# Kernel tuning notes

Measured on AMD Instinct MI355X. Metric: run time of the kernel, lower is better.

The kernel has to match this reference:

```python
import jax, jax.numpy as jnp
from jax import lax
import numpy as np

B, L, D_MODEL = 4, 2048, 1024
D_INNER = 2 * D_MODEL          # expand=2
N = 16                          # d_state
DCONV = 4                       # d_conv
DTRANK = D_MODEL // 16          # dt_rank = 64
DFF = 4 * D_MODEL               # 4096


def setup_inputs() -> dict:
    key = jax.random.key(0)
    ks = jax.random.split(key, 10)
    def g(i, shape, scale=0.02):
        return jax.random.normal(ks[i], shape, jnp.float32) * scale
    return {
        "x": jax.random.normal(ks[0], (B, L, D_MODEL), jnp.float32),
        # Mamba params (mamba_ssm defaults: in_proj/x_proj/out_proj no bias)
        "in_proj_w": g(1, (2 * D_INNER, D_MODEL)),
        "conv_w": g(2, (D_INNER, 1, DCONV), 0.1),
        "conv_b": jnp.zeros((D_INNER,), jnp.float32),
        "x_proj_w": g(3, (DTRANK + 2 * N, D_INNER)),
        "dt_proj_w": g(4, (D_INNER, DTRANK), 0.1),
        # inverse-softplus of ~0.01 so softplus(dt) starts small, as in Mamba init
        "dt_proj_b": jnp.log(jnp.expm1(jnp.full((D_INNER,), 1e-2, jnp.float32))),
        "A_log": jnp.log(jnp.broadcast_to(jnp.arange(1, N + 1, dtype=jnp.float32), (D_INNER, N))),
        "D": jnp.ones((D_INNER,), jnp.float32),
        "out_proj_w": g(5, (D_MODEL, D_INNER)),
        # FFN params (nn.Linear has bias)
        "lin1_w": g(6, (DFF, D_MODEL)),
        "lin1_b": jnp.zeros((DFF,), jnp.float32),
        "lin2_w": g(7, (D_MODEL, DFF)),
        "lin2_b": jnp.zeros((D_MODEL,), jnp.float32),
    }


def _mamba(x, in_proj_w, conv_w, conv_b, x_proj_w, dt_proj_w, dt_proj_b,
           A_log, D, out_proj_w):
    Bb = x.shape[0]
    xz = jnp.einsum('bld,ed->ble', x, in_proj_w)        # [B,L,2*d_inner]
    u, z = jnp.split(xz, 2, axis=-1)                    # each [B,L,d_inner]
    # causal depthwise conv1d over time
    uc = jnp.transpose(u, (0, 2, 1))                    # [B,d_inner,L]
    uc = lax.conv_general_dilated(uc, conv_w, (1,), [(DCONV - 1, 0)],
                                  feature_group_count=D_INNER)
    uc = jax.nn.silu(uc + conv_b[None, :, None])
    u = jnp.transpose(uc, (0, 2, 1))                    # [B,L,d_inner]
    # input-dependent dt, B, C
    x_dbl = jnp.einsum('ble,fe->blf', u, x_proj_w)      # [B,L,dt_rank+2N]
    dt, Bm, Cm = jnp.split(x_dbl, [DTRANK, DTRANK + N], axis=-1)
    dt = jax.nn.softplus(jnp.einsum('blr,er->ble', dt, dt_proj_w) + dt_proj_b)
    A = -jnp.exp(A_log)                                 # [d_inner,N]

    def step(h, inputs):
        u_t, dt_t, B_t, C_t = inputs                    # [B,E],[B,E],[B,N],[B,N]
        dA = jnp.exp(dt_t[..., None] * A)               # [B,E,N]
        h = dA * h + (dt_t * u_t)[..., None] * B_t[:, None, :]
        y = jnp.einsum('ben,bn->be', h, C_t)
        return h, y

    h0 = jnp.zeros((Bb, D_INNER, N), x.dtype)
    xs = (jnp.transpose(u, (1, 0, 2)), jnp.transpose(dt, (1, 0, 2)),
          jnp.transpose(Bm, (1, 0, 2)), jnp.transpose(Cm, (1, 0, 2)))
    _, ys = lax.scan(step, h0, xs)                      # ys: [L,B,d_inner]
    y = jnp.transpose(ys, (1, 0, 2)) + u * D
    y = y * jax.nn.silu(z)
    return jnp.einsum('ble,de->bld', y, out_proj_w)     # [B,L,d_model]


def reference(x, in_proj_w, conv_w, conv_b, x_proj_w, dt_proj_w, dt_proj_b,
              A_log, D, out_proj_w, lin1_w, lin1_b, lin2_w, lin2_b):
    y = _mamba(x, in_proj_w, conv_w, conv_b, x_proj_w, dt_proj_w, dt_proj_b,
               A_log, D, out_proj_w)
    h = jax.nn.relu(jnp.einsum('bld,fd->blf', y, lin1_w) + lin1_b)
    return jnp.einsum('blf,df->bld', h, lin2_w) + lin2_b
```

## Files before the change

### kernel.cpp

```cpp
#include <hip/hip_runtime.h>
#include <hip/hip_bf16.h>
#include <type_traits>
#include <math.h>

typedef __hip_bfloat16 bf16_t;

#define BB 4
#define LL 2048
#define DM 1024
#define DI 2048
#define NS 16
#define DTR 64
#define DFF 4096
#define MTOK (BB*LL)
#define NC 32
#define CL (LL/NC)
#define TT 16
#define KS 4

#if defined(__has_builtin)
#if __has_builtin(__builtin_amdgcn_exp2f)
#define EXP2F(x) __builtin_amdgcn_exp2f(x)
#endif
#endif
#ifndef EXP2F
#define EXP2F(x) exp2f(x)
#endif
#define LOG2E 1.44269504088896340736f

__device__ __forceinline__ float b2f_lo(unsigned u) {
    union { unsigned x; float f; } c; c.x = u << 16; return c.f;
}
__device__ __forceinline__ float b2f_hi(unsigned u) {
    union { unsigned x; float f; } c; c.x = u & 0xffff0000u; return c.f;
}
__device__ __forceinline__ void unpack8(uint4 v, float* o) {
    o[0] = b2f_lo(v.x); o[1] = b2f_hi(v.x);
    o[2] = b2f_lo(v.y); o[3] = b2f_hi(v.y);
    o[4] = b2f_lo(v.z); o[5] = b2f_hi(v.z);
    o[6] = b2f_lo(v.w); o[7] = b2f_hi(v.w);
}

typedef __attribute__((ext_vector_type(8))) short bf16x8;
typedef __attribute__((ext_vector_type(4))) float f32x4;

__device__ __forceinline__ void gld_lds16(const void* g, void* l) {
    __builtin_amdgcn_global_load_lds(
        (const __attribute__((address_space(1))) void*)g,
        (__attribute__((address_space(3))) void*)l, 16, 0, 0);
}

#define G8_BAR  __builtin_amdgcn_s_barrier()
#define G8_SB   __builtin_amdgcn_sched_barrier(0)
#define G8_LGKM do { asm volatile("s_waitcnt lgkmcnt(0)" ::: "memory"); G8_SB; } while (0)
#define G8_VM4  do { asm volatile("s_waitcnt vmcnt(4)"   ::: "memory"); G8_SB; } while (0)
#define G8_VM2  do { asm volatile("s_waitcnt vmcnt(2)"   ::: "memory"); G8_SB; } while (0)
#define G8_VM0  do { asm volatile("s_waitcnt vmcnt(0)"   ::: "memory"); G8_SB; } while (0)

__global__ void detect_dtype_kernel(const unsigned* __restrict__ x, int* __restrict__ flag)
{
    __shared__ int cnt;
    if (threadIdx.x == 0) cnt = 0;
    __syncthreads();
    int c = 0;
    for (int i = threadIdx.x; i < 4096; i += 256) {
        unsigned w = x[i];
        int e = (w >> 7) & 0xFF;
        c += (e >= 100 && e <= 140) ? 1 : 0;
    }
    atomicAdd(&cnt, c);
    __syncthreads();
    if (threadIdx.x == 0) *flag = (cnt > 2048) ? 1 : 0;
}

struct CvtDesc {
    const void* src[14];
    bf16_t*     dst[14];
    int         cum[15];
};

__global__ __launch_bounds__(256)
void convert_all(CvtDesc d, const int* __restrict__ flag, int total8)
{
    int i = blockIdx.x * 256 + threadIdx.x;
    if (i >= total8) return;
    int t = 0;
#pragma unroll 1
    while (i >= d.cum[t + 1]) ++t;
    int j = i - d.cum[t];
    if (*flag) {
        ((uint4*)d.dst[t])[j] = ((const uint4*)d.src[t])[j];
    } else {
        const float4* s = (const float4*)d.src[t] + (size_t)j * 2;
        float4 a = s[0], b = s[1];
        bf16_t o[8];
        o[0] = __float2bfloat16(a.x); o[1] = __float2bfloat16(a.y);
        o[2] = __float2bfloat16(a.z); o[3] = __float2bfloat16(a.w);
        o[4] = __float2bfloat16(b.x); o[5] = __float2bfloat16(b.y);
        o[6] = __float2bfloat16(b.z); o[7] = __float2bfloat16(b.w);
        ((uint4*)d.dst[t])[j] = *(uint4*)o;
    }
}

#define G8_NK 16

template <int EPI, bool SPLIT>
__global__ __launch_bounds__(512, 2)
void gemm8(const bf16_t* __restrict__ A, const bf16_t* __restrict__ W,
           bf16_t* __restrict__ C, bf16_t* __restrict__ C2,
           const bf16_t* __restrict__ bias, int ldc)
{
    __shared__ __align__(16) bf16_t ldsmem[2][2][256 * 64];

    const int tid  = threadIdx.x;
    const int lane = tid & 63;
    const int wv   = tid >> 6;
    const int wm   = wv >> 2;
    const int wn   = wv & 3;
    const int r16  = lane & 15;
    const int q    = lane >> 4;
    const int m0   = blockIdx.x * 256;
    const int n0   = blockIdx.y * 256;

    const int x0 = q ^ (r16 & 7);
    const int x1 = (4 + q) ^ (r16 & 7);

    const int srow = tid >> 3;
    const int scol = (tid & 7) ^ (srow & 7);
    const bf16_t* Abase = A + (size_t)(m0 + srow) * 1024 + scol * 8;
    const bf16_t* Wbase = W + (size_t)(n0 + srow) * 1024 + scol * 8;
    const int woff = wv * 1024;

    const bf16x8* L8 = (const bf16x8*)ldsmem;
    char*         Lb = (char*)ldsmem;

    f32x4  acc[8][4] = {};
    bf16x8 af[4][2];
    bf16x8 bfr[2][2][2];

    auto stA = [&](int bufc, int tile, int half) {
        const bf16_t* g = Abase + (size_t)half * (128 * 1024) + tile * 64;
        char* l = Lb + (size_t)(bufc * 2 + 0) * 32768 + half * 16384 + woff;
        gld_lds16(g, l);
        gld_lds16(g + 64 * 1024, l + 8192);
    };
    auto stB = [&](int bufc, int tile, int half) {
        const bf16_t* g = Wbase + (size_t)half * (128 * 1024) + tile * 64;
        char* l = Lb + (size_t)(bufc * 2 + 1) * 32768 + half * 16384 + woff;
        gld_lds16(g, l);
        gld_lds16(g + 64 * 1024, l + 8192);
    };
    auto rdA = [&](int bufc, int mh) {
#pragma unroll
        for (int mf = 0; mf < 4; ++mf) {
            int rb = (bufc * 2 + 0) * 2048 + (wm * 128 + mh * 64 + mf * 16 + r16) * 8;
            af[mf][0] = L8[rb + x0];
            af[mf][1] = L8[rb + x1];
        }
    };
    auto rdB = [&](int bufc, int nh) {
#pragma unroll
        for (int nf = 0; nf < 2; ++nf) {
            int rb = (bufc * 2 + 1) * 2048 + (wn * 64 + nh * 32 + nf * 16 + r16) * 8;
            bfr[nh][nf][0] = L8[rb + x0];
            bfr[nh][nf][1] = L8[rb + x1];
        }
    };
    auto mmQ = [&](int mh, int nh) {
#pragma unroll
        for (int mf = 0; mf < 4; ++mf)
#pragma unroll
            for (int nf = 0; nf < 2; ++nf) {
                acc[mh*4+mf][nh*2+nf] = __builtin_amdgcn_mfma_f32_16x16x32_bf16(
                    af[mf][0], bfr[nh][nf][0], acc[mh*4+mf][nh*2+nf], 0, 0, 0);
                acc[mh*4+mf][nh*2+nf] = __builtin_amdgcn_mfma_f32_16x16x32_bf16(
                    af[mf][1], bfr[nh][nf][1], acc[mh*4+mf][nh*2+nf], 0, 0, 0);
            }
    };

#define G8_PH(mh, nh) do { G8_BAR; G8_LGKM;                      \
        __builtin_amdgcn_s_setprio(1); mmQ(mh, nh);              \
        __builtin_amdgcn_s_setprio(0); G8_SB; G8_BAR; G8_SB; } while (0)

    stA(0, 0, 0); stA(0, 0, 1);
    stB(0, 0, 0); stB(0, 0, 1);
    stB(1, 1, 0); stB(1, 1, 1);
    G8_VM4;
    G8_BAR; G8_SB;

    for (int i = 0; i < G8_NK / 2 - 1; ++i) {
        const int v1 = 2 * i + 1, u2 = 2 * i + 2, v2 = 2 * i + 3;
        rdA(0,0); rdB(0,0); stA(1, v1, 0);         G8_PH(0,0);
        rdB(0,1);           stA(1, v1, 1);         G8_PH(0,1);
        rdA(0,1);           stB(0, u2, 0);         G8_PH(1,0);
                            stB(0, u2, 1); G8_VM4; G8_PH(1,1);
        rdA(1,0); rdB(1,0); stA(0, u2, 0);         G8_PH(0,0);
        rdB(1,1);           stA(0, u2, 1);         G8_PH(0,1);
        rdA(1,1);           stB(1, v2, 0);         G8_PH(1,0);
                            stB(1, v2, 1); G8_VM4; G8_PH(1,1);
    }
    rdA(0,0); rdB(0,0); stA(1, G8_NK - 1, 0); G8_PH(0,0);
    rdB(0,1);           stA(1, G8_NK - 1, 1); G8_PH(0,1);
    rdA(0,1);                                 G8_PH(1,0);
                        G8_VM0;               G8_PH(1,1);
    rdA(1,0); rdB(1,0);                       G8_PH(0,0);
    rdB(1,1);                                 G8_PH(0,1);
    rdA(1,1);                                 G8_PH(1,0);
                                              G8_PH(1,1);

    bf16_t* Cb = C;
    int csub = 0;
    if (SPLIT && n0 >= 2048) { Cb = C2; csub = 2048; }
#pragma unroll
    for (int b = 0; b < 4; ++b) {
        int colg = n0 + wn * 64 + (b >> 1) * 32 + (b & 1) * 16 + r16;
        float bv = 0.f;
        if (EPI >= 1) bv = __bfloat162float(bias[colg]);
#pragma unroll
        for (int a = 0; a < 8; ++a) {
#pragma unroll
            for (int r = 0; r < 4; ++r) {
                int rowg = m0 + wm * 128 + (a >> 2) * 64 + (a & 3) * 16 + q * 4 + r;
                float v = acc[a][b][r];
                if (EPI >= 1) v += bv;
                if (EPI == 2) v = v > 0.f ? v : 0.f;
                Cb[(size_t)rowg * ldc + (colg - csub)] = __float2bfloat16(v);
            }
        }
    }
#undef G8_PH
}

template <int LDK, int NKT, int EPI, bool DYN>
__global__ __launch_bounds__(512, 2)
void gemm8n(const bf16_t* __restrict__ A, const bf16_t* __restrict__ W,
            bf16_t* __restrict__ C, const bf16_t* __restrict__ bias, int ldc,
            const int* oflag, int c_row_off)
{
    __shared__ __align__(16) bf16_t ldsmem[2][24576];

    const int tid  = threadIdx.x;
    const int lane = tid & 63;
    const int wv   = tid >> 6;
    const int wm   = wv >> 2;
    const int wn   = wv & 3;
    const int r16  = lane & 15;
    const int q    = lane >> 4;
    const int m0   = blockIdx.x * 256;
    const int n0   = blockIdx.y * 128;

    const int x0 = q ^ (r16 & 7);
    const int x1 = (4 + q) ^ (r16 & 7);

    const int srow = tid >> 3;
    const int scol = (tid & 7) ^ (srow & 7);
    const bf16_t* Abase = A + (size_t)(m0 + srow) * LDK + scol * 8;
    const bf16_t* Wbase = W + (size_t)(n0 + srow) * LDK + scol * 8;
    const int woff = wv * 1024;

    const bf16x8* L8 = (const bf16x8*)ldsmem;
    char*         Lb = (char*)ldsmem;

    f32x4  acc[8][2] = {};
    bf16x8 af[4][2];
    bf16x8 bfr[2][2];

    auto stA = [&](int bufc, int tile, int half) {
        const bf16_t* g = Abase + (size_t)half * (128 * LDK) + tile * 64;
        char* l = Lb + (size_t)bufc * 49152 + half * 16384 + woff;
        gld_lds16(g, l);
        gld_lds16(g + (size_t)64 * LDK, l + 8192);
    };
    auto stB = [&](int bufc, int tile) {
        const bf16_t* g = Wbase + tile * 64;
        char* l = Lb + (size_t)bufc * 49152 + 32768 + woff;
        gld_lds16(g, l);
        gld_lds16(g + (size_t)64 * LDK, l + 8192);
    };
    auto rdA = [&](int bufc, int mh) {
#pragma unroll
        for (int mf = 0; mf < 4; ++mf) {
            int rb = bufc * 3072 + (wm * 128 + mh * 64 + mf * 16 + r16) * 8;
            af[mf][0] = L8[rb + x0];
            af[mf][1] = L8[rb + x1];
        }
    };
    auto rdB = [&](int bufc) {
#pragma unroll
        for (int nf = 0; nf < 2; ++nf) {
            int rb = bufc * 3072 + 2048 + (wn * 32 + nf * 16 + r16) * 8;
            bfr[nf][0] = L8[rb + x0];
            bfr[nf][1] = L8[rb + x1];
        }
    };
    auto mmP = [&](int mh) {
#pragma unroll
        for (int mf = 0; mf < 4; ++mf)
#pragma unroll
            for (int nf = 0; nf < 2; ++nf) {
                acc[mh*4+mf][nf] = __builtin_amdgcn_mfma_f32_16x16x32_bf16(
                    af[mf][0], bfr[nf][0], acc[mh*4+mf][nf], 0, 0, 0);
                acc[mh*4+mf][nf] = __builtin_amdgcn_mfma_f32_16x16x32_bf16(
                    af[mf][1], bfr[nf][1], acc[mh*4+mf][nf], 0, 0, 0);
            }
    };

#define GN_PH(mh) do { G8_BAR; G8_LGKM;                          \
        __builtin_amdgcn_s_setprio(1); mmP(mh);                  \
        __builtin_amdgcn_s_setprio(0); G8_SB; G8_BAR; G8_SB; } while (0)

    stA(0, 0, 0); stA(0, 0, 1);
    stB(0, 0);
    stB(1, 1);
    G8_VM2;
    G8_BAR; G8_SB;

    for (int i = 0; i < NKT / 2 - 1; ++i) {
        const int v1 = 2 * i + 1, u2 = 2 * i + 2, v2 = 2 * i + 3;
        rdA(0,0); rdB(0); stA(1, v1, 0); stA(1, v1, 1); GN_PH(0);
        rdA(0,1);         stB(0, u2); G8_VM2;           GN_PH(1);
        rdA(1,0); rdB(1); stA(0, u2, 0); stA(0, u2, 1); GN_PH(0);
        rdA(1,1);         stB(1, v2); G8_VM2;           GN_PH(1);
    }
    rdA(0,0); rdB(0); stA(1, NKT - 1, 0); stA(1, NKT - 1, 1); GN_PH(0);
    rdA(0,1);         G8_VM0;                                 GN_PH(1);
    rdA(1,0); rdB(1);                                         GN_PH(0);
    rdA(1,1);                                                 GN_PH(1);

    int of = 1;
    if constexpr (DYN) of = *oflag;
#pragma unroll
    for (int nf = 0; nf < 2; ++nf) {
        int colg = n0 + wn * 32 + nf * 16 + r16;
        float bv = 0.f;
        if (EPI >= 1) bv = __bfloat162float(bias[colg]);
#pragma unroll
        for (int a = 0; a < 8; ++a) {
#pragma unroll
            for (int r = 0; r < 4; ++r) {
                int rowg = m0 + wm * 128 + a * 16 + q * 4 + r;
                float v = acc[a][nf][r];
                if (EPI >= 1) v += bv;
                if constexpr (DYN) {
                    size_t idx = (size_t)(c_row_off + rowg) * ldc + colg;
                    if (of) ((bf16_t*)C)[idx] = __float2bfloat16(v);
                    else    ((float*)C)[idx]  = v;
                } else {
                    C[(size_t)rowg * ldc + colg] = __float2bfloat16(v);
                }
            }
        }
    }
#undef GN_PH
}

#define TM 128
#define TN 128
#define TK 64

template <typename OutT, int EPI, bool DYN, bool EDGE>
__global__ __launch_bounds__(256, 2)
void gemm_bt(const bf16_t* __restrict__ A, int lda,
             const bf16_t* __restrict__ W, int ldw,
             OutT* __restrict__ C, int ldc,
             OutT* __restrict__ C2, int nsplit,
             const bf16_t* __restrict__ bias,
             int M, int N, int K,
             const int* oflag, int c_row_off)
{
    __shared__ bf16_t sA[TM * TK];
    __shared__ bf16_t sB[TN * TK];

    const int tid  = threadIdx.x;
    const int lane = tid & 63;
    const int wv   = tid >> 6;
    const int m0   = blockIdx.x * TM;
    const int n0   = blockIdx.y * TN;
    const int wm   = (wv >> 1) * 64;
    const int wn   = (wv & 1) * 64;
    const int r16  = lane & 15;
    const int q    = lane >> 4;

    int of = 1;
    if constexpr (DYN) of = *oflag;

    f32x4 acc[4][4] = {};

    for (int k0 = 0; k0 < K; k0 += TK) {
#pragma unroll
        for (int i = 0; i < 4; ++i) {
            int c    = (i * 4 + wv) * 64 + lane;
            int row  = c >> 3;
            int col8 = c & 7;
            const bf16_t* ga = A + (size_t)(m0 + row) * lda + k0 + col8 * 8;
            gld_lds16(ga, (char*)sA + (size_t)(i * 4 + wv) * 1024);
            int nrow = n0 + row;
            if (EDGE && nrow > N - 1) nrow = N - 1;
            const bf16_t* gb = W + (size_t)nrow * ldw + k0 + col8 * 8;
            gld_lds16(gb, (char*)sB + (size_t)(i * 4 + wv) * 1024);
        }
        __syncthreads();

        const bf16x8* sA8 = (const bf16x8*)sA;
        const bf16x8* sB8 = (const bf16x8*)sB;
#pragma unroll
        for (int kk = 0; kk < 2; ++kk) {
            bf16x8 af[4], bfr[4];
#pragma unroll
            for (int i = 0; i < 4; ++i)
                af[i] = sA8[(wm + i * 16 + r16) * 8 + kk * 4 + q];
#pragma unroll
            for (int j = 0; j < 4; ++j)
                bfr[j] = sB8[(wn + j * 16 + r16) * 8 + kk * 4 + q];
#pragma unroll
            for (int i = 0; i < 4; ++i)
#pragma unroll
                for (int j = 0; j < 4; ++j)
                    acc[i][j] = __builtin_amdgcn_mfma_f32_16x16x32_bf16(
                        af[i], bfr[j], acc[i][j], 0, 0, 0);
        }
        __syncthreads();
    }

    OutT* Cb = C;
    int csub = 0;
    if (C2 != nullptr && n0 >= nsplit) { Cb = C2; csub = nsplit; }

#pragma unroll
    for (int j = 0; j < 4; ++j) {
        int colg = n0 + wn + j * 16 + r16;
        if (EDGE && colg >= N) continue;
        float bv = 0.f;
        if (EPI >= 1) bv = __bfloat162float(bias[colg]);
#pragma unroll
        for (int i = 0; i < 4; ++i) {
#pragma unroll
            for (int r = 0; r < 4; ++r) {
                int rowg = m0 + wm + i * 16 + q * 4 + r;
                if (EDGE && rowg >= M) continue;
                float v = acc[i][j][r];
                if (EPI >= 1) v += bv;
                if (EPI == 2) v = v > 0.f ? v : 0.f;
                if (EPI == 3) v = (v > 20.f) ? v : log1pf(__expf(v));
                if constexpr (DYN) {
                    size_t idx = (size_t)(c_row_off + rowg) * ldc + colg;
                    if (of) ((bf16_t*)Cb)[idx] = __float2bfloat16(v);
                    else    ((float*)Cb)[idx]  = v;
                } else if constexpr (std::is_same<OutT, float>::value) {
                    Cb[(size_t)rowg * ldc + (colg - csub)] = v;
                } else {
                    Cb[(size_t)rowg * ldc + (colg - csub)] = __float2bfloat16(v);
                }
            }
        }
    }
}

__global__ __launch_bounds__(256, 2)
void gemm_xproj_splitk(const bf16_t* __restrict__ A,
                       const bf16_t* __restrict__ W,
                       float* __restrict__ part, int M)
{
    __shared__ bf16_t sA[TM * TK];
    __shared__ bf16_t sB[TN * TK];

    const int tid  = threadIdx.x;
    const int lane = tid & 63;
    const int wv   = tid >> 6;
    const int m0   = blockIdx.x * TM;
    const int kz   = blockIdx.z;
    const int wm   = (wv >> 1) * 64;
    const int wn   = (wv & 1) * 64;
    const int r16  = lane & 15;
    const int q    = lane >> 4;

    f32x4 acc[4][4] = {};

    const int kbeg = kz * (2048 / KS);
    for (int k0 = kbeg; k0 < kbeg + 2048 / KS; k0 += TK) {
#pragma unroll
        for (int i = 0; i < 4; ++i) {
            int c    = (i * 4 + wv) * 64 + lane;
            int row  = c >> 3;
            int col8 = c & 7;
            const bf16_t* ga = A + (size_t)(m0 + row) * DI + k0 + col8 * 8;
            gld_lds16(ga, (char*)sA + (size_t)(i * 4 + wv) * 1024);
            int nrow = row; if (nrow > 95) nrow = 95;
            const bf16_t* gb = W + (size_t)nrow * DI + k0 + col8 * 8;
            gld_lds16(gb, (char*)sB + (size_t)(i * 4 + wv) * 1024);
        }
        __syncthreads();

        const bf16x8* sA8 = (const bf16x8*)sA;
        const bf16x8* sB8 = (const bf16x8*)sB;
#pragma unroll
        for (int kk = 0; kk < 2; ++kk) {
            bf16x8 af[4], bfr[4];
#pragma unroll
            for (int i = 0; i < 4; ++i)
                af[i] = sA8[(wm + i * 16 + r16) * 8 + kk * 4 + q];
#pragma unroll
            for (int j = 0; j < 4; ++j)
                bfr[j] = sB8[(wn + j * 16 + r16) * 8 + kk * 4 + q];
#pragma unroll
            for (int i = 0; i < 4; ++i)
#pragma unroll
                for (int j = 0; j < 4; ++j)
                    acc[i][j] = __builtin_amdgcn_mfma_f32_16x16x32_bf16(
                        af[i], bfr[j], acc[i][j], 0, 0, 0);
        }
        __syncthreads();
    }

#pragma unroll
    for (int j = 0; j < 4; ++j) {
        int colg = wn + j * 16 + r16;
        if (colg >= 96) continue;
#pragma unroll
        for (int i = 0; i < 4; ++i) {
#pragma unroll
            for (int r = 0; r < 4; ++r) {
                int rowg = m0 + wm + i * 16 + q * 4 + r;
                part[((size_t)kz * M + rowg) * 96 + colg] = acc[i][j][r];
            }
        }
    }
}

__global__ __launch_bounds__(256)
void xproj_reduce(const float* __restrict__ part, bf16_t* __restrict__ xdbl,
                  float* __restrict__ x32, int M)
{
    int i = blockIdx.x * 256 + threadIdx.x;
    int n = M * 96;
    if (i >= n) return;
    float s = part[i] + part[(size_t)n + i] + part[2 * (size_t)n + i] + part[3 * (size_t)n + i];
    xdbl[i] = __float2bfloat16(s);
    if (x32) x32[i] = s;
}

__global__ __launch_bounds__(256)
void conv_silu_kernel(const bf16_t* __restrict__ u,
                      const bf16_t* __restrict__ cw,
                      const bf16_t* __restrict__ cb,
                      bf16_t* __restrict__ uc,
                      int Mrows)
{
    int idx = blockIdx.x * 256 + threadIdx.x;
    int eg  = idx & 255;
    int row = idx >> 8;
    if (row >= Mrows) return;
    int t = row & (LL - 1);
    int b = row >> 11;
    int e0 = eg * 8;

    float wf[32];
    {
        const uint4* wp = (const uint4*)(cw + (size_t)e0 * 4);
        uint4 w0 = wp[0], w1 = wp[1], w2 = wp[2], w3 = wp[3];
        unpack8(w0, wf); unpack8(w1, wf + 8); unpack8(w2, wf + 16); unpack8(w3, wf + 24);
    }
    float bias[8];
    unpack8(*(const uint4*)(cb + e0), bias);

    float uk[4][8];
#pragma unroll
    for (int k = 0; k < 4; ++k) {
        int tt = t - 3 + k;
        if (tt >= 0) {
            uint4 uv = *(const uint4*)(u + (size_t)(b * LL + tt) * DI + e0);
            unpack8(uv, uk[k]);
        } else {
#pragma unroll
            for (int j = 0; j < 8; ++j) uk[k][j] = 0.f;
        }
    }
    bf16_t out8[8];
#pragma unroll
    for (int j = 0; j < 8; ++j) {
        float a = bias[j];
#pragma unroll
        for (int k = 0; k < 4; ++k) a += wf[j * 4 + k] * uk[k][j];
        a = a / (1.f + __expf(-a));
        out8[j] = __float2bfloat16(a);
    }
    *(uint4*)(uc + (size_t)row * DI + e0) = *(uint4*)out8;
}


__global__ __launch_bounds__(256, 2)
void scan_pass1(const bf16_t* __restrict__ uc, const bf16_t* __restrict__ dtb,
                const float* __restrict__ x32, const bf16_t* __restrict__ A_log,
                float* __restrict__ hfin, float* __restrict__ Ssum, int lgG)
{
    __shared__ __align__(16) char sm1[32768];
    const int tid  = threadIdx.x;
    const int lane = tid & 63;
    const int wv   = tid >> 6;
    const int bid  = blockIdx.x;
    const int eb   = bid & 7;
    const int rem  = bid >> 3;
    const int b    = rem & ((1 << lgG) - 1);
    const int chunk = rem >> lgG;
    const int e0   = eb * 256;
    const int e    = e0 + tid;
    const int t0   = chunk * CL;

    float alf[16];
    {
        uint4 v0 = *(const uint4*)(A_log + (size_t)e * NS);
        uint4 v1 = *(const uint4*)(A_log + (size_t)e * NS + 8);
        unpack8(v0, alf); unpack8(v1, alf + 8);
    }
    float a0 = -__expf(alf[0]) * LOG2E;
    float Aa2[16];
    int fast = 1;
#pragma unroll
    for (int n = 0; n < 16; ++n) {
        Aa2[n] = -__expf(alf[n]) * LOG2E;
        float ideal = (float)(n + 1) * a0;
        fast = fast && (fabsf(Aa2[n] - ideal) <= 0.02f * fabsf(ideal));
    }
    int allfast = __syncthreads_and(fast);

    const bf16_t* ub = uc  + (size_t)(b * LL + t0) * DI;
    const bf16_t* db = dtb + (size_t)(b * LL + t0) * DI;
    const float*  xr = x32 + (size_t)(b * LL + t0) * 96 + 64;

    char* const U[2] = { sm1, sm1 + 8192 };
    char* const D[2] = { sm1 + 16384, sm1 + 24576 };

    auto stage2 = [&](const bf16_t* src, char* dst, int trow0) {
        const int c8 = (lane & 31) * 8;
        const int r0 = 2 * wv + (lane >> 5);
        gld_lds16(src + (size_t)(trow0 + r0) * DI + e0 + c8, dst + wv * 1024 + lane * 16);
        gld_lds16(src + (size_t)(trow0 + r0 + 8) * DI + e0 + c8, dst + (wv + 4) * 1024 + lane * 16);
    };

    float h[16];
#pragma unroll
    for (int j = 0; j < 16; ++j) h[j] = 0.f;
    float Ss = 0.f;

    stage2(ub, U[0], 0);  stage2(db, D[0], 0);
    stage2(ub, U[1], TT); stage2(db, D[1], TT);

#define P1_TILE(K, FAST) do {                                               \
        asm volatile("s_waitcnt vmcnt(0)" ::: "memory"); G8_SB;             \
        __builtin_amdgcn_s_barrier(); G8_SB;                                \
        { const char* Ut = U[(K) & 1]; const char* Dt = D[(K) & 1];         \
          const float* bct = xr + (size_t)(K) * TT * 96;                    \
          _Pragma("unroll")                                                 \
          for (int t = 0; t < TT; ++t) {                                    \
              float cu  = __bfloat162float(*(const bf16_t*)(Ut + t * 512 + tid * 2)); \
              float cdt = __bfloat162float(*(const bf16_t*)(Dt + t * 512 + tid * 2)); \
              const float* bc = bct + t * 96;                               \
              float du = cdt * cu; Ss += cdt;                               \
              if (FAST) {                                                   \
                  float r = EXP2F(cdt * a0);                                \
                  float r2 = r * r, r4 = r2 * r2, r8 = r4 * r4;             \
                  float dA = r, dB = r8 * r;                                \
                  _Pragma("unroll")                                         \
                  for (int j = 0; j < 8; ++j) { h[j] = dA * h[j] + du * bc[j]; dA *= r; } \
                  _Pragma("unroll")                                         \
                  for (int j = 8; j < 16; ++j) { h[j] = dB * h[j] + du * bc[j]; dB *= r; } \
              } else {                                                      \
                  _Pragma("unroll")                                         \
                  for (int j = 0; j < 16; ++j) {                            \
                      float dA = EXP2F(cdt * Aa2[j]);                       \
                      h[j] = dA * h[j] + du * bc[j]; }                      \
              }                                                             \
          } }                                                               \
        asm volatile("s_waitcnt lgkmcnt(0)" ::: "memory"); G8_SB;           \
        __builtin_amdgcn_s_barrier(); G8_SB;                                \
        if ((K) + 2 < CL / TT) {                                            \
            stage2(ub, U[(K) & 1], ((K) + 2) * TT);                         \
            stage2(db, D[(K) & 1], ((K) + 2) * TT);                         \
        }                                                                   \
    } while (0)

    if (allfast) { P1_TILE(0, true);  P1_TILE(1, true);  P1_TILE(2, true);  P1_TILE(3, true); }
    else         { P1_TILE(0, false); P1_TILE(1, false); P1_TILE(2, false); P1_TILE(3, false); }
#undef P1_TILE

    size_t base = (size_t)(b * NC + chunk) * NS * DI + e;
#pragma unroll
    for (int j = 0; j < 16; ++j) hfin[base + (size_t)j * DI] = h[j];
    Ssum[(size_t)(b * NC + chunk) * DI + e] = Ss;
}

__global__ __launch_bounds__(256)
void scan_pass2(const float* __restrict__ Ssum, const bf16_t* __restrict__ A_log,
                float* __restrict__ hfin)
{
    int idx = blockIdx.x * 256 + threadIdx.x;
    int e = idx & (DI - 1);
    int rem = idx >> 11;
    int n = rem & (NS - 1);
    int b = rem >> 4;
    float Aa2 = -__expf(__bfloat162float(A_log[(size_t)e * NS + n])) * LOG2E;
    float h = 0.f;
    for (int c = 0; c < NC; ++c) {
        size_t a = ((size_t)(b * NC + c) * NS + n) * DI + e;
        float S  = Ssum[(size_t)(b * NC + c) * DI + e];
        float hf = hfin[a];
        hfin[a] = h;
        h = EXP2F(Aa2 * S) * h + hf;
    }
}

__global__ __launch_bounds__(256, 2)
void scan_pass3(const bf16_t* __restrict__ uc, const bf16_t* __restrict__ dtb,
                const float* __restrict__ x32, bf16_t* __restrict__ zy,
                const bf16_t* __restrict__ A_log, const bf16_t* __restrict__ Dp,
                const float* __restrict__ hin, int lgG)
{
    __shared__ __align__(16) char sm3[57344];
    const int tid  = threadIdx.x;
    const int lane = tid & 63;
    const int wv   = tid >> 6;
    const int bid  = blockIdx.x;
    const int eb   = bid & 7;
    const int rem  = bid >> 3;
    const int b    = rem & ((1 << lgG) - 1);
    const int chunk = rem >> lgG;
    const int e0   = eb * 256;
    const int e    = e0 + tid;
    const int t0   = chunk * CL;

    float alf[16];
    {
        uint4 v0 = *(const uint4*)(A_log + (size_t)e * NS);
        uint4 v1 = *(const uint4*)(A_log + (size_t)e * NS + 8);
        unpack8(v0, alf); unpack8(v1, alf + 8);
    }
    float a0 = -__expf(alf[0]) * LOG2E;
    float Aa2[16];
    int fast = 1;
#pragma unroll
    for (int n = 0; n < 16; ++n) {
        Aa2[n] = -__expf(alf[n]) * LOG2E;
        float ideal = (float)(n + 1) * a0;
        fast = fast && (fabsf(Aa2[n] - ideal) <= 0.02f * fabsf(ideal));
    }
    int allfast = __syncthreads_and(fast);

    float Dv = __bfloat162float(Dp[e]);
    size_t hbase = (size_t)(b * NC + chunk) * NS * DI + e;
    float h[16];
#pragma unroll
    for (int j = 0; j < 16; ++j) h[j] = hin[hbase + (size_t)j * DI];

    const bf16_t* ub = uc  + (size_t)(b * LL + t0) * DI;
    const bf16_t* db = dtb + (size_t)(b * LL + t0) * DI;
    bf16_t*       zb = zy  + (size_t)(b * LL + t0) * DI;
    const float*  xr = x32 + (size_t)(b * LL + t0) * 96 + 64;

    char* const U[2] = { sm3, sm3 + 8192 };
    char* const D[2] = { sm3 + 16384, sm3 + 24576 };
    char* const Z[2] = { sm3 + 32768, sm3 + 40960 };
    char* const Y    = sm3 + 49152;

    auto stage2 = [&](const bf16_t* src, char* dst, int trow0) {
        const int c8 = (lane & 31) * 8;
        const int r0 = 2 * wv + (lane >> 5);
        gld_lds16(src + (size_t)(trow0 + r0) * DI + e0 + c8, dst + wv * 1024 + lane * 16);
        gld_lds16(src + (size_t)(trow0 + r0 + 8) * DI + e0 + c8, dst + (wv + 4) * 1024 + lane * 16);
    };
    auto yflush = [&](int K) {
        const int r0 = tid >> 5;
        const int c  = (tid & 31) * 16;
        uint4 v0 = *(const uint4*)(Y + r0 * 512 + c);
        uint4 v1 = *(const uint4*)(Y + (r0 + 8) * 512 + c);
        *(uint4*)(zb + (size_t)(K * TT + r0) * DI + e0 + (tid & 31) * 8)     = v0;
        *(uint4*)(zb + (size_t)(K * TT + r0 + 8) * DI + e0 + (tid & 31) * 8) = v1;
    };

    stage2(ub, U[0], 0);  stage2(db, D[0], 0);  stage2(zb, Z[0], 0);
    stage2(ub, U[1], TT); stage2(db, D[1], TT); stage2(zb, Z[1], TT);

#define P3_TILE(K, FAST) do {                                               \
        asm volatile("s_waitcnt vmcnt(0)" ::: "memory"); G8_SB;             \
        __builtin_amdgcn_s_barrier(); G8_SB;                                \
        { const char* Ut = U[(K) & 1]; const char* Dt = D[(K) & 1];         \
          const char* Zt = Z[(K) & 1];                                      \
          const float* bct = xr + (size_t)(K) * TT * 96;                    \
          _Pragma("unroll")                                                 \
          for (int t = 0; t < TT; ++t) {                                    \
              float cu  = __bfloat162float(*(const bf16_t*)(Ut + t * 512 + tid * 2)); \
              float cdt = __bfloat162float(*(const bf16_t*)(Dt + t * 512 + tid * 2)); \
              float cz  = __bfloat162float(*(const bf16_t*)(Zt + t * 512 + tid * 2)); \
              const float* bc = bct + t * 96;                               \
              float du = cdt * cu;                                          \
              if (FAST) {                                                   \
                  float r = EXP2F(cdt * a0);                                \
                  float r2 = r * r, r4 = r2 * r2, r8 = r4 * r4;             \
                  float dA = r, dB = r8 * r;                                \
                  _Pragma("unroll")                                         \
                  for (int j = 0; j < 8; ++j) { h[j] = dA * h[j] + du * bc[j]; dA *= r; } \
                  _Pragma("unroll")                                         \
                  for (int j = 8; j < 16; ++j) { h[j] = dB * h[j] + du * bc[j]; dB *= r; } \
              } else {                                                      \
                  _Pragma("unroll")                                         \
                  for (int j = 0; j < 16; ++j) {                            \
                      float dA = EXP2F(cdt * Aa2[j]);                       \
                      h[j] = dA * h[j] + du * bc[j]; }                      \
              }                                                             \
              float y1 = 0.f, y2 = 0.f;                                     \
              _Pragma("unroll")                                             \
              for (int j = 0; j < 8; ++j)  y1 += h[j] * bc[16 + j];         \
              _Pragma("unroll")                                             \
              for (int j = 8; j < 16; ++j) y2 += h[j] * bc[16 + j];         \
              float yv  = y1 + y2;                                          \
              float sil = cz / (1.f + __expf(-cz));                         \
              *(bf16_t*)(Y + t * 512 + tid * 2) =                           \
                  __float2bfloat16((yv + cu * Dv) * sil);                   \
          } }                                                               \
        asm volatile("s_waitcnt lgkmcnt(0)" ::: "memory"); G8_SB;           \
        __builtin_amdgcn_s_barrier(); G8_SB;                                \
        yflush(K);                                                          \
        if ((K) + 2 < CL / TT) {                                            \
            stage2(ub, U[(K) & 1], ((K) + 2) * TT);                         \
            stage2(db, D[(K) & 1], ((K) + 2) * TT);                         \
            stage2(zb, Z[(K) & 1], ((K) + 2) * TT);                         \
        }                                                                   \
    } while (0)

    if (allfast) { P3_TILE(0, true);  P3_TILE(1, true);  P3_TILE(2, true);  P3_TILE(3, true); }
    else         { P3_TILE(0, false); P3_TILE(1, false); P3_TILE(2, false); P3_TILE(3, false); }
#undef P3_TILE
}

__global__ __launch_bounds__(64)
void scan_kernel(const bf16_t* __restrict__ uc,
                 const bf16_t* __restrict__ dt,
                 const bf16_t* __restrict__ xdbl,
                 bf16_t* __restrict__ zy,
                 const bf16_t* __restrict__ A_log,
                 const bf16_t* __restrict__ Dp)
{
    int idx = blockIdx.x * 64 + threadIdx.x;
    int e = idx & (DI - 1);
    int b = idx >> 11;

    float Aa[NS];
#pragma unroll
    for (int n = 0; n < NS; ++n)
        Aa[n] = -__expf(__bfloat162float(A_log[e * NS + n]));
    float Dv = __bfloat162float(Dp[e]);
    float h[NS];
#pragma unroll
    for (int n = 0; n < NS; ++n) h[n] = 0.f;

    const bf16_t* up  = uc   + (size_t)b * LL * DI + e;
    const bf16_t* dp  = dt   + (size_t)b * LL * DI + e;
    const bf16_t* zp  = zy   + (size_t)b * LL * DI + e;
    const bf16_t* bcp = xdbl + (size_t)b * LL * 96 + 64;
    bf16_t*       yp  = zy   + (size_t)b * LL * DI + e;

    float nu  = __bfloat162float(*up);
    float ndt = __bfloat162float(*dp);
    float nz  = __bfloat162float(*zp);
    uint4 nb0 = *(const uint4*)(bcp);
    uint4 nb1 = *(const uint4*)(bcp + 8);
    uint4 nc0 = *(const uint4*)(bcp + 16);
    uint4 nc1 = *(const uint4*)(bcp + 24);

    for (int t = 0; t < LL; ++t) {
        float cu = nu, cdt = ndt, cz = nz;
        uint4 b0 = nb0, b1 = nb1, c0 = nc0, c1 = nc1;
        if (t + 1 < LL) {
            up += DI; dp += DI; zp += DI; bcp += 96;
            nu  = __bfloat162float(*up);
            ndt = __bfloat162float(*dp);
            nz  = __bfloat162float(*zp);
            nb0 = *(const uint4*)(bcp);
            nb1 = *(const uint4*)(bcp + 8);
            nc0 = *(const uint4*)(bcp + 16);
            nc1 = *(const uint4*)(bcp + 24);
        }
        float Bv[NS], Cv[NS];
        unpack8(b0, Bv); unpack8(b1, Bv + 8);
        unpack8(c0, Cv); unpack8(c1, Cv + 8);

        float du = cdt * cu;
        float yv = 0.f;
#pragma unroll
        for (int n = 0; n < NS; ++n) {
            float dA = __expf(cdt * Aa[n]);
            h[n] = dA * h[n] + du * Bv[n];
            yv += h[n] * Cv[n];
        }
        float sil  = cz / (1.f + __expf(-cz));
        float outv = (yv + cu * Dv) * sil;
        *yp = __float2bfloat16(outv);
        yp += DI;
    }
}

extern "C" void kernel_launch(void* const* d_in, const int* in_sizes, int n_in,
                              void* d_out, int out_size, void* d_ws, size_t ws_size,
                              hipStream_t stream)
{
    char* ws = (char*)d_ws;
    int* flag = (int*)ws;
    size_t cur = 256;
    auto alloc = [&](size_t bytes) { bf16_t* p = (bf16_t*)(ws + cur); cur += bytes; return p; };

    const size_t o_xb = cur;
    bf16_t* xb   = alloc((size_t)MTOK * DM * 2);
    bf16_t* w_in = alloc((size_t)2 * DI * DM * 2);
    bf16_t* w_o  = alloc((size_t)DM * DI * 2);
    bf16_t* w_l1 = alloc((size_t)DFF * DM * 2);
    bf16_t* w_l2 = alloc((size_t)DM * DFF * 2);
    bf16_t* w_xp = alloc((size_t)96 * DI * 2);
    bf16_t* w_dt = alloc((size_t)DI * DTR * 2);
    bf16_t* cw   = alloc((size_t)DI * 4 * 2);
    bf16_t* cb   = alloc((size_t)DI * 2);
    bf16_t* dpb  = alloc((size_t)DI * 2);
    bf16_t* alog = alloc((size_t)DI * NS * 2);
    bf16_t* dd   = alloc((size_t)DI * 2);
    bf16_t* l1b  = alloc((size_t)DFF * 2);
    bf16_t* l2b  = alloc((size_t)DM * 2 + 2048);
    cur = (cur + 255) & ~(size_t)255;
    const size_t o_pipe = cur;

    detect_dtype_kernel<<<1, 256, 0, stream>>>((const unsigned*)d_in[0], flag);

    {
        CvtDesc d;
        const void* ss[14] = { d_in[0], d_in[1], d_in[9], d_in[10], d_in[12], d_in[4],
                               d_in[5], d_in[2], d_in[3], d_in[6], d_in[7], d_in[8],
                               d_in[11], d_in[13] };
        bf16_t* dd_[14]    = { xb, w_in, w_o, w_l1, w_l2, w_xp,
                               w_dt, cw, cb, dpb, alog, dd, l1b, l2b };
        size_t  nn[14]     = { (size_t)MTOK*DM, (size_t)2*DI*DM, (size_t)DM*DI,
                               (size_t)DFF*DM, (size_t)DM*DFF, (size_t)96*DI,
                               (size_t)DI*DTR, (size_t)DI*4, (size_t)DI, (size_t)DI,
                               (size_t)DI*NS, (size_t)DI, (size_t)DFF, (size_t)DM };
        int c = 0; d.cum[0] = 0;
        for (int i = 0; i < 14; ++i) {
            d.src[i] = ss[i]; d.dst[i] = dd_[i];
            c += (int)(nn[i] / 8); d.cum[i + 1] = c;
        }
        convert_all<<<(c + 255) / 256, 256, 0, stream>>>(d, flag, c);
    }

    auto pipe = [&](int Gq) { return (size_t)Gq * LL * 96 * 2 + 3ull * Gq * LL * DI * 2; };
    auto scr  = [&](int Gq) {
        return (size_t)Gq * NC * NS * DI * 4 + (size_t)Gq * NC * DI * 4 + (size_t)Gq * LL * 96 * 4;
    };

    int G; bool chunked; size_t scr_off;
    if      (ws_size >= o_pipe + pipe(4))            { G = 4; chunked = true;  scr_off = o_xb; }
    else if (ws_size >= o_pipe + pipe(2) + scr(2))   { G = 2; chunked = true;  scr_off = o_pipe + pipe(2); }
    else if (ws_size >= o_pipe + pipe(1) + scr(1))   { G = 1; chunked = true;  scr_off = o_pipe + pipe(1); }
    else                                             { G = 1; chunked = false; scr_off = o_pipe + pipe(1); }
    const int lgG = (G == 4) ? 2 : (G == 2 ? 1 : 0);

    const size_t hfin_sz = (size_t)G * NC * NS * DI * 4;
    const size_t ssum_sz = (size_t)G * NC * DI * 4;

    for (int g0 = 0; g0 < BB; g0 += G) {
        const int    Mg      = G * LL;
        const size_t xdbl_sz = (size_t)Mg * 96 * 2;
        const size_t big     = (size_t)Mg * DI * 2;

        bf16_t* xdbl = (bf16_t*)(ws + o_pipe);
        bf16_t* ubuf = (bf16_t*)(ws + o_pipe + xdbl_sz);
        bf16_t* dtb  = ubuf;
        bf16_t* zbuf = (bf16_t*)(ws + o_pipe + xdbl_sz + big);
        bf16_t* uc   = (bf16_t*)(ws + o_pipe + xdbl_sz + 2 * big);
        bf16_t* my   = uc;
        bf16_t* hh   = (bf16_t*)(ws + o_pipe);
        float*  xpp  = (float*)(ws + scr_off);
        float*  x32  = chunked ? (float*)(ws + scr_off + hfin_sz + ssum_sz) : nullptr;

        const bf16_t* x_g = xb + (size_t)g0 * LL * DM;

        dim3 blk(256);
        const int gx = Mg / TM;

        gemm8<0, true><<<dim3(Mg / 256, 16), 512, 0, stream>>>(
            x_g, w_in, ubuf, zbuf, nullptr, DI);
        conv_silu_kernel<<<Mg, 256, 0, stream>>>(ubuf, cw, cb, uc, Mg);
        gemm_xproj_splitk<<<dim3(gx, 1, KS), blk, 0, stream>>>(uc, w_xp, xpp, Mg);
        xproj_reduce<<<(Mg * 96 + 255) / 256, 256, 0, stream>>>(xpp, xdbl, x32, Mg);
        gemm_bt<bf16_t, 3, false, false><<<dim3(gx, DI / TN), blk, 0, stream>>>(
            xdbl, 96, w_dt, DTR, dtb, DI, nullptr, 0, dpb, Mg, DI, DTR, nullptr, 0);
        if (chunked) {
            float* hfin = (float*)(ws + scr_off);
            float* Ssum = (float*)(ws + scr_off + hfin_sz);
            scan_pass1<<<G * NC * (DI / 256), 256, 0, stream>>>(uc, dtb, x32, alog, hfin, Ssum, lgG);
            scan_pass2<<<G * (NS * DI / 256), 256, 0, stream>>>(Ssum, alog, hfin);
            scan_pass3<<<G * NC * (DI / 256), 256, 0, stream>>>(uc, dtb, x32, zbuf, alog, dd, hfin, lgG);
        } else {
            scan_kernel<<<(G * DI) / 64, 64, 0, stream>>>(uc, dtb, xdbl, zbuf, alog, dd);
        }
        gemm8n<2048, 32, 0, false><<<dim3(Mg / 256, DM / 128), 512, 0, stream>>>(
            zbuf, w_o, my, nullptr, DM, nullptr, 0);
        gemm8<2, false><<<dim3(Mg / 256, 16), 512, 0, stream>>>(
            my, w_l1, hh, nullptr, l1b, DFF);
        gemm8n<4096, 64, 1, true><<<dim3(Mg / 256, DM / 128), 512, 0, stream>>>(
            hh, w_l2, (bf16_t*)d_out, l2b, DM, (const int*)ws, g0 * LL);
    }
}
```

Measured before the change: 674.2 us.

## Stage B/C into LDS and use partial vmcnt waits in scan passes

Both chunked-scan kernels now copy their per-chunk B (and C) vectors from global memory into LDS with async global-to-LDS loads issued before the A_log setup. The tile loop is rewritten as an explicit sequence that waits with partial vmcnt counts, so the next tile's prefetch keeps flowing while the current tile computes, instead of draining all loads every tile. Pass1 also raises the launch-bounds occupancy hint from 2 to 4 blocks. The intent is to remove repeated global reads of B/C in the inner loop and the full-drain stalls. The cost is extra LDS per block and fragile hand-counted waitcnt values that must match the order loads are issued.

```diff
diff --git a/kernel.cpp b/kernel.cpp
--- a/kernel.cpp
+++ b/kernel.cpp
@@ -53,6 +53,8 @@
 #define G8_BAR  __builtin_amdgcn_s_barrier()
 #define G8_SB   __builtin_amdgcn_sched_barrier(0)
 #define G8_LGKM do { asm volatile("s_waitcnt lgkmcnt(0)" ::: "memory"); G8_SB; } while (0)
+#define G8_VM8  do { asm volatile("s_waitcnt vmcnt(8)"   ::: "memory"); G8_SB; } while (0)
+#define G8_VM6  do { asm volatile("s_waitcnt vmcnt(6)"   ::: "memory"); G8_SB; } while (0)
 #define G8_VM4  do { asm volatile("s_waitcnt vmcnt(4)"   ::: "memory"); G8_SB; } while (0)
 #define G8_VM2  do { asm volatile("s_waitcnt vmcnt(2)"   ::: "memory"); G8_SB; } while (0)
 #define G8_VM0  do { asm volatile("s_waitcnt vmcnt(0)"   ::: "memory"); G8_SB; } while (0)
@@ -588,12 +590,12 @@
 }
 
 
-__global__ __launch_bounds__(256, 2)
+__global__ __launch_bounds__(256, 4)
 void scan_pass1(const bf16_t* __restrict__ uc, const bf16_t* __restrict__ dtb,
                 const float* __restrict__ x32, const bf16_t* __restrict__ A_log,
                 float* __restrict__ hfin, float* __restrict__ Ssum, int lgG)
 {
-    __shared__ __align__(16) char sm1[32768];
+    __shared__ __align__(16) char sm1[36864];
     const int tid  = threadIdx.x;
     const int lane = tid & 63;
     const int wv   = tid >> 6;
@@ -606,6 +608,27 @@
     const int e    = e0 + tid;
     const int t0   = chunk * CL;
 
+    const bf16_t* ub = uc  + (size_t)(b * LL + t0) * DI;
+    const bf16_t* db = dtb + (size_t)(b * LL + t0) * DI;
+    const float*  xr = x32 + (size_t)(b * LL + t0) * 96 + 64;
+
+    char* const U[2] = { sm1, sm1 + 8192 };
+    char* const D[2] = { sm1 + 16384, sm1 + 24576 };
+    char* const Bl   = sm1 + 32768;
+
+    auto stage2 = [&](const bf16_t* src, char* dst, int trow0) {
+        const int c8 = (lane & 31) * 8;
+        const int r0 = 2 * wv + (lane >> 5);
+        gld_lds16(src + (size_t)(trow0 + r0) * DI + e0 + c8, dst + wv * 1024 + lane * 16);
+        gld_lds16(src + (size_t)(trow0 + r0 + 8) * DI + e0 + c8, dst + (wv + 4) * 1024 + lane * 16);
+    };
+    {
+        int s = tid >> 2, p = tid & 3;
+        gld_lds16(xr + (size_t)s * 96 + p * 4, Bl + tid * 16);
+    }
+    stage2(ub, U[0], 0);  stage2(db, D[0], 0);
+    stage2(ub, U[1], TT); stage2(db, D[1], TT);
+
     float alf[16];
     {
         uint4 v0 = *(const uint4*)(A_log + (size_t)e * NS);
@@ -623,65 +646,51 @@
     }
     int allfast = __syncthreads_and(fast);
 
-    const bf16_t* ub = uc  + (size_t)(b * LL + t0) * DI;
-    const bf16_t* db = dtb + (size_t)(b * LL + t0) * DI;
-    const float*  xr = x32 + (size_t)(b * LL + t0) * 96 + 64;
-
-    char* const U[2] = { sm1, sm1 + 8192 };
-    char* const D[2] = { sm1 + 16384, sm1 + 24576 };
-
-    auto stage2 = [&](const bf16_t* src, char* dst, int trow0) {
-        const int c8 = (lane & 31) * 8;
-        const int r0 = 2 * wv + (lane >> 5);
-        gld_lds16(src + (size_t)(trow0 + r0) * DI + e0 + c8, dst + wv * 1024 + lane * 16);
-        gld_lds16(src + (size_t)(trow0 + r0 + 8) * DI + e0 + c8, dst + (wv + 4) * 1024 + lane * 16);
-    };
-
     float h[16];
 #pragma unroll
     for (int j = 0; j < 16; ++j) h[j] = 0.f;
     float Ss = 0.f;
 
-    stage2(ub, U[0], 0);  stage2(db, D[0], 0);
-    stage2(ub, U[1], TT); stage2(db, D[1], TT);
-
-#define P1_TILE(K, FAST) do {                                               \
-        asm volatile("s_waitcnt vmcnt(0)" ::: "memory"); G8_SB;             \
-        __builtin_amdgcn_s_barrier(); G8_SB;                                \
-        { const char* Ut = U[(K) & 1]; const char* Dt = D[(K) & 1];         \
-          const float* bct = xr + (size_t)(K) * TT * 96;                    \
-          _Pragma("unroll")                                                 \
-          for (int t = 0; t < TT; ++t) {                                    \
-              float cu  = __bfloat162float(*(const bf16_t*)(Ut + t * 512 + tid * 2)); \
-              float cdt = __bfloat162float(*(const bf16_t*)(Dt + t * 512 + tid * 2)); \
-              const float* bc = bct + t * 96;                               \
-              float du = cdt * cu; Ss += cdt;                               \
-              if (FAST) {                                                   \
-                  float r = EXP2F(cdt * a0);                                \
-                  float r2 = r * r, r4 = r2 * r2, r8 = r4 * r4;             \
-                  float dA = r, dB = r8 * r;                                \
-                  _Pragma("unroll")                                         \
-                  for (int j = 0; j < 8; ++j) { h[j] = dA * h[j] + du * bc[j]; dA *= r; } \
-                  _Pragma("unroll")                                         \
-                  for (int j = 8; j < 16; ++j) { h[j] = dB * h[j] + du * bc[j]; dB *= r; } \
-              } else {                                                      \
-                  _Pragma("unroll")                                         \
-                  for (int j = 0; j < 16; ++j) {                            \
-                      float dA = EXP2F(cdt * Aa2[j]);                       \
-                      h[j] = dA * h[j] + du * bc[j]; }                      \
-              }                                                             \
-          } }                                                               \
-        asm volatile("s_waitcnt lgkmcnt(0)" ::: "memory"); G8_SB;           \
-        __builtin_amdgcn_s_barrier(); G8_SB;                                \
-        if ((K) + 2 < CL / TT) {                                            \
-            stage2(ub, U[(K) & 1], ((K) + 2) * TT);                         \
-            stage2(db, D[(K) & 1], ((K) + 2) * TT);                         \
-        }                                                                   \
+#define P1_CMP(K, FAST) do {                                                  \
+        const char* Ut = U[(K) & 1]; const char* Dt = D[(K) & 1];             \
+        _Pragma("unroll")                                                     \
+        for (int t = 0; t < TT; ++t) {                                        \
+            float cu  = __bfloat162float(*(const bf16_t*)(Ut + t * 512 + tid * 2)); \
+            float cdt = __bfloat162float(*(const bf16_t*)(Dt + t * 512 + tid * 2)); \
+            const float* bc = (const float*)(Bl + ((K) * TT + t) * 64);       \
+            float du = cdt * cu; Ss += cdt;                                   \
+            if (FAST) {                                                       \
+                float r = EXP2F(cdt * a0);                                    \
+                float r2 = r * r, r4 = r2 * r2, r8 = r4 * r4;                 \
+                float dA = r, dB = r8 * r;                                    \
+                _Pragma("unroll")                                             \
+                for (int j = 0; j < 8; ++j) { h[j] = dA * h[j] + du * bc[j]; dA *= r; } \
+                _Pragma("unroll")                                             \
+                for (int j = 8; j < 16; ++j) { h[j] = dB * h[j] + du * bc[j]; dB *= r; } \
+            } else {                                                          \
+                _Pragma("unroll")                                             \
+                for (int j = 0; j < 16; ++j) {                                \
+                    float dA = EXP2F(cdt * Aa2[j]);                           \
+                    h[j] = dA * h[j] + du * bc[j]; }                          \
+            }                                                                 \
+        } } while (0)
+
+#define P1_SEQ(FAST) do {                                                     \
+        G8_VM4; G8_BAR; G8_SB;                                                \
+        P1_CMP(0, FAST); G8_LGKM; G8_BAR; G8_SB;                              \
+        stage2(ub, U[0], 2 * TT); stage2(db, D[0], 2 * TT);                   \
+        G8_VM4; G8_BAR; G8_SB;                                                \
+        P1_CMP(1, FAST); G8_LGKM; G8_BAR; G8_SB;                              \
+        stage2(ub, U[1], 3 * TT); stage2(db, D[1], 3 * TT);                   \
+        G8_VM4; G8_BAR; G8_SB;                                                \
+        P1_CMP(2, FAST); G8_LGKM; G8_BAR; G8_SB;                              \
+        G8_VM0; G8_BAR; G8_SB;                                                \
+        P1_CMP(3, FAST);                                                      \
     } while (0)
 
-    if (allfast) { P1_TILE(0, true);  P1_TILE(1, true);  P1_TILE(2, true);  P1_TILE(3, true); }
-    else         { P1_TILE(0, false); P1_TILE(1, false); P1_TILE(2, false); P1_TILE(3, false); }
-#undef P1_TILE
+    if (allfast) P1_SEQ(true); else P1_SEQ(false);
+#undef P1_SEQ
+#undef P1_CMP
 
     size_t base = (size_t)(b * NC + chunk) * NS * DI + e;
 #pragma unroll
@@ -715,7 +724,7 @@
                 const bf16_t* __restrict__ A_log, const bf16_t* __restrict__ Dp,
                 const float* __restrict__ hin, int lgG)
 {
-    __shared__ __align__(16) char sm3[57344];
+    __shared__ __align__(16) char sm3[65536];
     const int tid  = threadIdx.x;
     const int lane = tid & 63;
     const int wv   = tid >> 6;
@@ -728,6 +737,31 @@
     const int e    = e0 + tid;
     const int t0   = chunk * CL;
 
+    const bf16_t* ub = uc  + (size_t)(b * LL + t0) * DI;
+    const bf16_t* db = dtb + (size_t)(b * LL + t0) * DI;
+    bf16_t*       zb = zy  + (size_t)(b * LL + t0) * DI;
+    const float*  xr = x32 + (size_t)(b * LL + t0) * 96 + 64;
+
+    char* const U[2] = { sm3, sm3 + 8192 };
+    char* const D[2] = { sm3 + 16384, sm3 + 24576 };
+    char* const Z[2] = { sm3 + 32768, sm3 + 40960 };
+    char* const Y    = sm3 + 49152;
+    char* const BC   = sm3 + 57344;
+
+    auto stage2 = [&](const bf16_t* src, char* dst, int trow0) {
+        const int c8 = (lane & 31) * 8;
+        const int r0 = 2 * wv + (lane >> 5);
+        gld_lds16(src + (size_t)(trow0 + r0) * DI + e0 + c8, dst + wv * 1024 + lane * 16);
+        gld_lds16(src + (size_t)(trow0 + r0 + 8) * DI + e0 + c8, dst + (wv + 4) * 1024 + lane * 16);
+    };
+    {
+        int s1 = tid >> 3, p1 = tid & 7;
+        gld_lds16(xr + (size_t)s1 * 96 + p1 * 4, BC + tid * 16);
+        gld_lds16(xr + (size_t)(s1 + 32) * 96 + p1 * 4, BC + 4096 + tid * 16);
+    }
+    stage2(ub, U[0], 0);  stage2(db, D[0], 0);  stage2(zb, Z[0], 0);
+    stage2(ub, U[1], TT); stage2(db, D[1], TT); stage2(zb, Z[1], TT);
+
     float alf[16];
     {
         uint4 v0 = *(const uint4*)(A_log + (size_t)e * NS);
@@ -751,22 +785,6 @@
 #pragma unroll
     for (int j = 0; j < 16; ++j) h[j] = hin[hbase + (size_t)j * DI];
 
-    const bf16_t* ub = uc  + (size_t)(b * LL + t0) * DI;
-    const bf16_t* db = dtb + (size_t)(b * LL + t0) * DI;
-    bf16_t*       zb = zy  + (size_t)(b * LL + t0) * DI;
-    const float*  xr = x32 + (size_t)(b * LL + t0) * 96 + 64;
-
-    char* const U[2] = { sm3, sm3 + 8192 };
-    char* const D[2] = { sm3 + 16384, sm3 + 24576 };
-    char* const Z[2] = { sm3 + 32768, sm3 + 40960 };
-    char* const Y    = sm3 + 49152;
-
-    auto stage2 = [&](const bf16_t* src, char* dst, int trow0) {
-        const int c8 = (lane & 31) * 8;
-        const int r0 = 2 * wv + (lane >> 5);
-        gld_lds16(src + (size_t)(trow0 + r0) * DI + e0 + c8, dst + wv * 1024 + lane * 16);
-        gld_lds16(src + (size_t)(trow0 + r0 + 8) * DI + e0 + c8, dst + (wv + 4) * 1024 + lane * 16);
-    };
     auto yflush = [&](int K) {
         const int r0 = tid >> 5;
         const int c  = (tid & 31) * 16;
@@ -776,59 +794,61 @@
         *(uint4*)(zb + (size_t)(K * TT + r0 + 8) * DI + e0 + (tid & 31) * 8) = v1;
     };
 
-    stage2(ub, U[0], 0);  stage2(db, D[0], 0);  stage2(zb, Z[0], 0);
-    stage2(ub, U[1], TT); stage2(db, D[1], TT); stage2(zb, Z[1], TT);
-
-#define P3_TILE(K, FAST) do {                                               \
-        asm volatile("s_waitcnt vmcnt(0)" ::: "memory"); G8_SB;             \
-        __builtin_amdgcn_s_barrier(); G8_SB;                                \
-        { const char* Ut = U[(K) & 1]; const char* Dt = D[(K) & 1];         \
-          const char* Zt = Z[(K) & 1];                                      \
-          const float* bct = xr + (size_t)(K) * TT * 96;                    \
-          _Pragma("unroll")                                                 \
-          for (int t = 0; t < TT; ++t) {                                    \
-              float cu  = __bfloat162float(*(const bf16_t*)(Ut + t * 512 + tid * 2)); \
-              float cdt = __bfloat162float(*(const bf16_t*)(Dt + t * 512 + tid * 2)); \
-              float cz  = __bfloat162float(*(const bf16_t*)(Zt + t * 512 + tid * 2)); \
-              const float* bc = bct + t * 96;                               \
-              float du = cdt * cu;                                          \
-              if (FAST) {                                                   \
-                  float r = EXP2F(cdt * a0);                                \
-                  float r2 = r * r, r4 = r2 * r2, r8 = r4 * r4;             \
-                  float dA = r, dB = r8 * r;                                \
-                  _Pragma("unroll")                                         \
-                  for (int j = 0; j < 8; ++j) { h[j] = dA * h[j] + du * bc[j]; dA *= r; } \
-                  _Pragma("unroll")                                         \
-                  for (int j = 8; j < 16; ++j) { h[j] = dB * h[j] + du * bc[j]; dB *= r; } \
-              } else {                                                      \
-                  _Pragma("unroll")                                         \
-                  for (int j = 0; j < 16; ++j) {                            \
-                      float dA = EXP2F(cdt * Aa2[j]);                       \
-                      h[j] = dA * h[j] + du * bc[j]; }                      \
-              }                                                             \
-              float y1 = 0.f, y2 = 0.f;                                     \
-              _Pragma("unroll")                                             \
-              for (int j = 0; j < 8; ++j)  y1 += h[j] * bc[16 + j];         \
-              _Pragma("unroll")                                             \
-              for (int j = 8; j < 16; ++j) y2 += h[j] * bc[16 + j];         \
-              float yv  = y1 + y2;                                          \
-              float sil = cz / (1.f + __expf(-cz));                         \
-              *(bf16_t*)(Y + t * 512 + tid * 2) =                           \
-                  __float2bfloat16((yv + cu * Dv) * sil);                   \
-          } }                                                               \
-        asm volatile("s_waitcnt lgkmcnt(0)" ::: "memory"); G8_SB;           \
-        __builtin_amdgcn_s_barrier(); G8_SB;                                \
-        yflush(K);                                                          \
-        if ((K) + 2 < CL / TT) {                                            \
-            stage2(ub, U[(K) & 1], ((K) + 2) * TT);                         \
-            stage2(db, D[(K) & 1], ((K) + 2) * TT);                         \
-            stage2(zb, Z[(K) & 1], ((K) + 2) * TT);                         \
-        }                                                                   \
+#define P3_CMP(K, FAST) do {                                                  \
+        const char* Ut = U[(K) & 1]; const char* Dt = D[(K) & 1];             \
+        const char* Zt = Z[(K) & 1];                                          \
+        _Pragma("unroll")                                                     \
+        for (int t = 0; t < TT; ++t) {                                        \
+            float cu  = __bfloat162float(*(const bf16_t*)(Ut + t * 512 + tid * 2)); \
+            float cdt = __bfloat162float(*(const bf16_t*)(Dt + t * 512 + tid * 2)); \
+            float cz  = __bfloat162float(*(const bf16_t*)(Zt + t * 512 + tid * 2)); \
+            const float* bc = (const float*)(BC + ((K) * TT + t) * 128);      \
+            float du = cdt * cu;                                              \
+            if (FAST) {                                                       \
+                float r = EXP2F(cdt * a0);                                    \
+                float r2 = r * r, r4 = r2 * r2, r8 = r4 * r4;                 \
+                float dA = r, dB = r8 * r;                                    \
+                _Pragma("unroll")                                             \
+                for (int j = 0; j < 8; ++j) { h[j] = dA * h[j] + du * bc[j]; dA *= r; } \
+                _Pragma("unroll")                                             \
+                for (int j = 8; j < 16; ++j) { h[j] = dB * h[j] + du * bc[j]; dB *= r; } \
+            } else {                                                          \
+                _Pragma("unroll")                                             \
+                for (int j = 0; j < 16; ++j) {                                \
+                    float dA = EXP2F(cdt * Aa2[j]);                           \
+                    h[j] = dA * h[j] + du * bc[j]; }                          \
+            }                                                                 \
+            float y1 = 0.f, y2 = 0.f;                                         \
+            _Pragma("unroll")                                                 \
+            for (int j = 0; j < 8; ++j)  y1 += h[j] * bc[16 + j];             \
+            _Pragma("unroll")                                                 \
+            for (int j = 8; j < 16; ++j) y2 += h[j] * bc[16 + j];             \
+            float yv  = y1 + y2;                                              \
+            float sil = cz / (1.f + __expf(-cz));                             \
+            *(bf16_t*)(Y + t * 512 + tid * 2) =                               \
+                __float2bfloat16((yv + cu * Dv) * sil);                       \
+        } } while (0)
+
+#define P3_SEQ(FAST) do {                                                     \
+        G8_VM6; G8_BAR; G8_SB;                                                \
+        P3_CMP(0, FAST); G8_LGKM; G8_BAR; G8_SB;                              \
+        yflush(0);                                                            \
+        stage2(ub, U[0], 2*TT); stage2(db, D[0], 2*TT); stage2(zb, Z[0], 2*TT); \
+        G8_VM8; G8_BAR; G8_SB;                                                \
+        P3_CMP(1, FAST); G8_LGKM; G8_BAR; G8_SB;                              \
+        yflush(1);                                                            \
+        stage2(ub, U[1], 3*TT); stage2(db, D[1], 3*TT); stage2(zb, Z[1], 3*TT); \
+        G8_VM8; G8_BAR; G8_SB;                                                \
+        P3_CMP(2, FAST); G8_LGKM; G8_BAR; G8_SB;                              \
+        yflush(2);                                                            \
+        G8_VM2; G8_BAR; G8_SB;                                                \
+        P3_CMP(3, FAST); G8_LGKM; G8_BAR; G8_SB;                              \
+        yflush(3);                                                            \
     } while (0)
 
-    if (allfast) { P3_TILE(0, true);  P3_TILE(1, true);  P3_TILE(2, true);  P3_TILE(3, true); }
-    else         { P3_TILE(0, false); P3_TILE(1, false); P3_TILE(2, false); P3_TILE(3, false); }
-#undef P3_TILE
+    if (allfast) P3_SEQ(true); else P3_SEQ(false);
+#undef P3_SEQ
+#undef P3_CMP
 }
 
 __global__ __launch_bounds__(64)
```

Measured after the change: 630.8 us. 1.07x faster.
